# Optimization experiments

Hardware: AMD Instinct MI355X
Metric: run time of the kernel (lower is better)

The kernel has to match this reference:

```python
import jax, jax.numpy as jnp
import numpy as np

PRECS = 1e-6
# [min, max] scaling ranges for the 12 XAJ parameters (order matches parameters[:, i, :])
PARA_SCALE = [[0.3, 2.0], [0.0, 5.0], [0.01, 100.0], [0.01, 100.0], [0.01, 200.0],
              [0.09, 1.0], [0.01, 100.0], [0.0, 10.0], [0.01, 0.7], [0.01, 0.7],
              [0.0, 0.998], [0.0, 0.998]]


def setup_inputs() -> dict:
    key = jax.random.key(0)
    k1, k2 = jax.random.split(key)
    Nstep, Ngrid, mu = 365, 2000, 8
    # col 0 = P (mm/d), col 2 = PET (mm/d); col 1 unused by the model
    x = jax.random.uniform(k1, (Nstep, Ngrid, 3), dtype=jnp.float32) * 10.0
    parameters = jax.random.uniform(k2, (Ngrid, 12, mu), dtype=jnp.float32)
    return {"x": x, "parameters": parameters, "mu": mu}


def _xaj(x, parameters, mu):
    P = x[:, :, 0]          # [T, Ngrid]
    PET = x[:, :, 2]        # [T, Ngrid]  (index 2, matching the original code)
    Ngrid = x.shape[1]

    sc = lambda a, i: PARA_SCALE[i][0] + a * (PARA_SCALE[i][1] - PARA_SCALE[i][0])
    (parKE, parB, parWUM, parWLM, parWM, parC, parSM, parEX,
     parKI_, parKG_, parCI, parCG) = [sc(parameters[:, i, :], i) for i in range(12)]

    wdm = jnp.maximum(parWM - parWUM - parWLM, 0.0)
    sum_k = parKI_ + parKG_
    parKI = jnp.where(sum_k < 1.0, parKI_, (1.0 - PRECS) * parKI_ / (sum_k + PRECS))
    parKG = jnp.where(sum_k < 1.0, parKG_, (1.0 - PRECS) * parKG_ / (sum_k + PRECS))

    init_state = jnp.full((Ngrid, mu), 0.001, dtype=jnp.float32)
    WU0 = WL0 = WD0 = S0 = QI0 = QG0 = FR0_init = init_state

    def step(carry, inp):
        WU, WL, WD, S, FR0, QI, QG = carry
        P_row, PET_row = inp                      # each [Ngrid]
        P_t = P_row[:, None]                      # broadcast over mu
        PET_t = PET_row[:, None] * parKE

        # three-layer evapotranspiration
        EU = jnp.minimum(PET_t, WU + P_t)
        D = jnp.maximum(PET_t - EU, 0.0)
        wet_excess = jnp.maximum(WL - parC * parWLM, 0.0)
        wet_ratio = wet_excess / (wet_excess + 1.0)
        EL_wet = D * WL / (parWLM + PRECS)
        EL_dry = jnp.minimum(parC * D, WL)
        EL = jnp.maximum(wet_ratio * EL_wet + (1.0 - wet_ratio) * EL_dry, 0.0)
        EL = jnp.minimum(EL, WL)
        D_res = jnp.maximum(D - EL, 0.0)
        ED = jnp.minimum(parC * D_res, WD)
        E = EU + EL + ED

        # saturation-excess runoff
        PE = jnp.maximum(P_t - E, 0.0)
        W = WU + WL + WD
        WMM = parWM * (1.0 + parB)
        base_W = jnp.maximum(1.0 - W / (parWM + PRECS), PRECS)
        A = WMM * (1.0 - base_W ** (1.0 / (1.0 + parB)))
        ratio = jnp.minimum((PE + A) / (WMM + PRECS), 1.0)
        R_per = jnp.where(PE + A < WMM,
                          PE - (parWM - W) + parWM * (1.0 - ratio) ** (1.0 + parB),
                          PE - (parWM - W))
        R_per = jnp.maximum(R_per, 0.0)

        # soil moisture update (fill top-down, deplete top-down)
        dW = P_t - E - R_per
        dpos = jnp.maximum(dW, 0.0)
        fill_u = jnp.minimum(dpos, jnp.maximum(parWUM - WU, 0.0))
        WU = WU + fill_u; dpos = dpos - fill_u
        fill_l = jnp.minimum(dpos, jnp.maximum(parWLM - WL, 0.0))
        WL = WL + fill_l; dpos = dpos - fill_l
        fill_d = jnp.minimum(dpos, jnp.maximum(wdm - WD, 0.0))
        WD = WD + fill_d
        dneg = jnp.maximum(-dW, 0.0)
        sub_u = jnp.minimum(dneg, WU)
        WU = WU - sub_u; dneg = dneg - sub_u
        sub_l = jnp.minimum(dneg, WL)
        WL = WL - sub_l; dneg = dneg - sub_l
        sub_d = jnp.minimum(dneg, WD)
        WD = WD - sub_d

        # free-water reservoir + three-flow separation
        FR_new = R_per / (PE + PRECS)
        FR = jnp.where(PE > 0.0, FR_new, FR0)
        FR = jnp.clip(FR, 0.0, 1.0)
        S_eq = jnp.minimum(S * FR0 / (FR + PRECS), parSM)
        SMM = parSM * (1.0 + parEX)
        ratio_s = jnp.maximum(1.0 - S_eq / (parSM + PRECS), PRECS)
        AU = SMM * (1.0 - ratio_s ** (1.0 / (1.0 + parEX)))
        ratio_pa = jnp.minimum((PE + AU) / (SMM + PRECS), 1.0)
        RS1 = (PE + S_eq - parSM + parSM * (1.0 - ratio_pa) ** (1.0 + parEX)) * FR
        RS2 = (PE + S_eq - parSM) * FR
        RS = jnp.where(PE + AU < SMM, RS1, RS2)
        RS = jnp.minimum(jnp.maximum(RS, 0.0), R_per)
        S = jnp.minimum(S_eq + (R_per - RS) / (FR + PRECS), parSM)
        RI = parKI * S * FR
        RG = parKG * S * FR
        S = S * (1.0 - parKI - parKG)

        # linear reservoirs
        QI = parCI * QI + (1.0 - parCI) * RI
        QG = parCG * QG + (1.0 - parCG) * RG

        return (WU, WL, WD, S, FR, QI, QG), (RS, QI, QG, E)

    carry0 = (WU0, WL0, WD0, S0, FR0_init, QI0, QG0)
    _, (QS_inflow, QI_inflow, QG_inflow, ET_series) = jax.lax.scan(step, carry0, (P, PET))

    QSave = QS_inflow.mean(-1, keepdims=True)
    QIave = QI_inflow.mean(-1, keepdims=True)
    QGave = QG_inflow.mean(-1, keepdims=True)
    ETave = ET_series.mean(-1, keepdims=True)
    river_inflow = QS_inflow + QI_inflow + QG_inflow
    Qs = river_inflow.mean(-1, keepdims=True)   # muwts is None
    # [Nstep, Ngrid, 5]
    return jnp.concatenate([Qs, QSave, QIave, QGave, ETave], axis=-1)


def reference(x, parameters, mu):
    return _xaj(x, parameters, mu)
```

## Files before the change

### kernel.cpp

```cpp
#include <hip/hip_runtime.h>

#define PRECS 1e-6f

__device__ __forceinline__ float fpow(float b, float e) {
    return __builtin_amdgcn_exp2f(e * __builtin_amdgcn_logf(b));
}

__device__ __forceinline__ float frcp(float v) {
    return __builtin_amdgcn_rcpf(v);
}

template <int CTRL>
__device__ __forceinline__ float dpp_mov(float v) {
    return __int_as_float(
        __builtin_amdgcn_update_dpp(0, __float_as_int(v), CTRL, 0xF, 0xF, true));
}

__device__ __forceinline__ float rsum8(float v) {
    v += dpp_mov<0xB1>(v);
    v += dpp_mov<0x4E>(v);
    v += dpp_mov<0x141>(v);
    return v;
}

__global__ __launch_bounds__(192, 1) void xaj_kernel(
    const float* __restrict__ x,
    const float* __restrict__ prm,
    float* __restrict__ out)
{
    constexpr int Nstep = 365, Ngrid = 2000;
    constexpr int xstride = Ngrid * 3;
    constexpr int K = 16;
    constexpr int NBLK = 23;

    const int wid  = (int)threadIdx.x >> 6;
    const int lane = (int)threadIdx.x & 63;
    const int g = blockIdx.x * 8 + (lane >> 3);
    const int m = lane & 7;

    __shared__ float2 stIn[2][K][64];
    __shared__ float4 stA[2][K][64];
    __shared__ float4 stB[2][K][64];

    const float lo[12] = {0.3f,0.0f,0.01f,0.01f,0.01f,0.09f,0.01f,0.0f,0.01f,0.01f,0.0f,0.0f};
    const float hi[12] = {2.0f,5.0f,100.0f,100.0f,200.0f,1.0f,100.0f,10.0f,0.7f,0.7f,0.998f,0.998f};
    float p[12];
    const float* pb = prm + (size_t)g * 96 + m;
#pragma unroll
    for (int i = 0; i < 12; ++i)
        p[i] = lo[i] + pb[i * 8] * (hi[i] - lo[i]);

    const float KE=p[0], B=p[1], WUM=p[2], WLM=p[3], WM=p[4], C=p[5],
                SM=p[6], EX=p[7], KI_=p[8], KG_=p[9], CI=p[10], CG=p[11];

    const float wdm  = fmaxf(WM - WUM - WLM, 0.f);
    const float sumk = KI_ + KG_;
    const float nrm  = (1.f - PRECS) / (sumk + PRECS);
    const float KI   = (sumk < 1.f) ? KI_ : KI_ * nrm;
    const float KG   = (sumk < 1.f) ? KG_ : KG_ * nrm;
    const float expB = 1.f + B,  invB  = 1.f / expB;
    const float WMM  = WM * expB;
    const float expEX= 1.f + EX, invEX = 1.f / expEX;
    const float SMM  = SM * expEX;
    const float inv_WLM = 1.f / (WLM + PRECS);
    const float inv_WM  = 1.f / (WM  + PRECS);
    const float inv_WMM = 1.f / (WMM + PRECS);
    const float inv_SM  = 1.f / (SM  + PRECS);
    const float inv_SMM = 1.f / (SMM + PRECS);
    const float oneK = 1.f - KI - KG;
    const float omCI = 1.f - CI, omCG = 1.f - CG;
    const float CWLM = C * WLM;
    const float inv1p = 1.f / (1.f + PRECS);
    const float eps2  = fmaxf(PRECS, fmaf(-SM, inv_SM, 1.f));

    float WU = 0.001f, WL = 0.001f, WD = 0.001f;
    float S = 0.001f, FR0 = 0.001f;
    float iFR0 = frcp(FR0 + PRECS);
    float QI = 0.001f, QG = 0.001f;
    const float cKI = omCI * KI, cKG = omCG * KG;
    const float wa = (m == 0 || m == 1) ? 0.125f : 0.f;
    const float wb = (m == 0 || m == 2) ? 0.125f : 0.f;
    const float wc = (m == 0 || m == 3) ? 0.125f : 0.f;
    const float wd = (m >= 4) ? 0.125f : 0.f;
    const int   col = (m < 4) ? m : 4;
    float* outp = out + (size_t)g * 5 + col;
    const size_t ostr = (size_t)Ngrid * 5;
    const float* xg = x + (size_t)g * 3;
    float Pr[K], Er[K];

    auto ASTEP = [&](int buf) {
        float2 rin[K];
#pragma unroll
        for (int k = 0; k < K; ++k)
            rin[k] = stIn[buf][k][lane];
#pragma unroll
        for (int k = 0; k < K; ++k) {
            const float Pt = rin[k].x, PET_t = rin[k].y;
            const float EU = fminf(PET_t, WU + Pt);
            const float D  = fmaxf(PET_t - Pt - WU, 0.f);
            const float we = fmaxf(WL - CWLM, 0.f);
            const float wr = we * frcp(we + 1.f);
            const float cwet = wr * WL * inv_WLM;
            const float ELdry = fminf(C * D, WL);
            const float EL = fminf(fmaxf(fmaf(1.f - wr, ELdry, cwet * D), 0.f), WL);
            const float ED = fminf(C * fmaxf(D - EL, 0.f), WD);
            const float E  = EU + EL + ED;
            const float PE = fmaxf(Pt - E, 0.f);
            const float W = WU + WL + WD;
            const float base_W = fmaxf(fmaf(-W, inv_WM, 1.f), PRECS);
            const float pw1 = fpow(base_W, invB);
            const float omr = fmaxf(fmaf(-PE, inv_WMM, pw1), 0.f);
            const float R_per = fmaxf(fmaf(WM, fpow(omr, expB), PE + (W - WM)), 0.f);
            const float dW = Pt - E - R_per;
            const float capD = fmaxf(wdm, WD);
            const float cum0 = WU + dW;
            const float WUn  = __builtin_amdgcn_fmed3f(cum0, 0.f, WUM);
            const float cum1 = WL + (cum0 - WUn);
            const float WLn  = __builtin_amdgcn_fmed3f(cum1, 0.f, WLM);
            const float cum2 = WD + (cum1 - WLn);
            const float WDn  = __builtin_amdgcn_fmed3f(cum2, 0.f, capD);
            WU = WUn; WL = WLn; WD = WDn;
            stA[buf][k][lane] = make_float4(PE, R_per, E, 0.f);
        }
    };

    auto BSTEP = [&](int buf) {
        float4 ra[K];
#pragma unroll
        for (int k = 0; k < K; ++k)
            ra[k] = stA[buf][k][lane];
        float FRn[K], iFRn[K];
#pragma unroll
        for (int k = 0; k < K; ++k) {
            const float q  = frcp(ra[k].x + PRECS);
            const float aa = ra[k].y * q;
            FRn[k]  = fminf(aa, 1.f);
            iFRn[k] = fmaxf(frcp(aa + PRECS), inv1p);
        }
#pragma unroll
        for (int k = 0; k < K; ++k) {
            const float PE = ra[k].x, R_per = ra[k].y;
            const bool wet = PE > 0.f;
            const float FR  = wet ? FRn[k]  : FR0;
            const float iFR = wet ? iFRn[k] : iFR0;
            const float sf  = S * FR0;
            const float sf2 = sf * inv_SM;
            const float S_eq = fminf(sf * iFR, SM);
            const float ratio_s = fmaxf(fmaf(-sf2, iFR, 1.f), eps2);
            const float u   = fpow(ratio_s, invEX);
            const float om2 = fmaxf(fmaf(-PE, inv_SMM, u), 0.f);
            const float base = (PE - SM) + S_eq;
            float RS = fmaf(SM, fpow(om2, expEX), base) * FR;
            RS = __builtin_amdgcn_fmed3f(RS, 0.f, R_per);
            const float Sn = fminf(fmaf(R_per - RS, iFR, S_eq), SM);
            S  = Sn * oneK;
            FR0 = FR; iFR0 = iFR;
            stB[buf][k][lane] = make_float4(RS, FR * Sn, ra[k].z, 0.f);
        }
    };

    auto CISSUE = [&](int blk) {
#pragma unroll
        for (int k = 0; k < K; ++k) {
            int t = blk * K + k;
            t = (t < Nstep) ? t : Nstep - 1;
            const float* xq = xg + (size_t)t * xstride;
            Pr[k] = xq[0];
            Er[k] = xq[2];
        }
    };
    auto CWRITE = [&](int buf) {
#pragma unroll
        for (int k = 0; k < K; ++k)
            stIn[buf][k][lane] = make_float2(Pr[k], Er[k] * KE);
    };
    auto CRED = [&](int buf, int q) {
        float4 rb[K];
#pragma unroll
        for (int k = 0; k < K; ++k)
            rb[k] = stB[buf][k][lane];
        const int t0 = q * K;
#pragma unroll
        for (int k = 0; k < K; ++k) {
            QI = fmaf(CI, QI, cKI * rb[k].y);
            QG = fmaf(CG, QG, cKG * rb[k].y);
            const float u0 = rsum8(rb[k].x);
            const float u1 = rsum8(QI);
            const float u2 = rsum8(QG);
            const float u3 = rsum8(rb[k].z);
            const float v = fmaf(u0, wa, fmaf(u1, wb, fmaf(u2, wc, u3 * wd)));
            if (t0 + k < Nstep)
                outp[(size_t)(t0 + k) * ostr] = v;
        }
    };

    if (wid == 2) { CISSUE(0); CWRITE(0); }
    __syncthreads();

#pragma unroll 1
    for (int i = 0; i < 13; ++i) {
        const int p0 = 2 * i, p1 = 2 * i + 1;
        if (wid == 0) {
            if (p0 < NBLK) ASTEP(0);
        } else if (wid == 1) {
            if (p0 >= 1 && p0 <= NBLK) BSTEP(1);
        } else {
            const bool ld = (p0 + 1 < NBLK);
            if (ld) CISSUE(p0 + 1);
            if (p0 >= 2) CRED(0, p0 - 2);
            if (ld) CWRITE(1);
        }
        __syncthreads();
        if (wid == 0) {
            if (p1 < NBLK) ASTEP(1);
        } else if (wid == 1) {
            if (p1 <= NBLK) BSTEP(0);
        } else {
            const bool ld = (p1 + 1 < NBLK);
            if (ld) CISSUE(p1 + 1);
            if (p1 >= 2) CRED(1, p1 - 2);
            if (ld) CWRITE(0);
        }
        __syncthreads();
    }
}

extern "C" void kernel_launch(void* const* d_in, const int* in_sizes, int n_in,
                              void* d_out, int out_size, void* d_ws, size_t ws_size,
                              hipStream_t stream) {
    const float* x   = (const float*)d_in[0];
    const float* prm = (const float*)d_in[1];
    float* out = (float*)d_out;
    xaj_kernel<<<250, 192, 0, stream>>>(x, prm, out);
}
```

Measured before the change: 58.07 us.

## Split pipeline into four warp-specialized stages with dedicated FR precompute wave

Adds a fourth wavefront so the pipeline runs A (soil moisture), FR precompute plus input load, B (free water), and D (reservoir routing, reductions, stores) as separate stages. FR/iFR precomputation moves out of the serial B stage into the loader wave, and the output reduction moves to its own wave. This shortens the critical serial B stage. The cost is a deeper pipeline with more phases and a 4-deep stA buffer, more shared memory, and one more wave per block.

```diff
diff --git a/kernel.cpp b/kernel.cpp
--- a/kernel.cpp
+++ b/kernel.cpp
@@ -23,7 +23,7 @@
     return v;
 }
 
-__global__ __launch_bounds__(192, 1) void xaj_kernel(
+__global__ __launch_bounds__(256, 1) void xaj_kernel(
     const float* __restrict__ x,
     const float* __restrict__ prm,
     float* __restrict__ out)
@@ -32,6 +32,7 @@
     constexpr int xstride = Ngrid * 3;
     constexpr int K = 16;
     constexpr int NBLK = 23;
+    constexpr int NPH  = NBLK + 3;
 
     const int wid  = (int)threadIdx.x >> 6;
     const int lane = (int)threadIdx.x & 63;
@@ -39,8 +40,9 @@
     const int m = lane & 7;
 
     __shared__ float2 stIn[2][K][64];
-    __shared__ float4 stA[2][K][64];
-    __shared__ float4 stB[2][K][64];
+    __shared__ float4 stA[4][K][64];
+    __shared__ float2 stFR[2][K][64];
+    __shared__ float2 stB[2][K][64];
 
     const float lo[12] = {0.3f,0.0f,0.01f,0.01f,0.01f,0.09f,0.01f,0.0f,0.01f,0.01f,0.0f,0.0f};
     const float hi[12] = {2.0f,5.0f,100.0f,100.0f,200.0f,1.0f,100.0f,10.0f,0.7f,0.7f,0.998f,0.998f};
@@ -88,7 +90,7 @@
     const float* xg = x + (size_t)g * 3;
     float Pr[K], Er[K];
 
-    auto ASTEP = [&](int buf) {
+    auto ASTEP = [&](int buf, int obuf) {
         float2 rin[K];
 #pragma unroll
         for (int k = 0; k < K; ++k)
@@ -120,29 +122,23 @@
             const float cum2 = WD + (cum1 - WLn);
             const float WDn  = __builtin_amdgcn_fmed3f(cum2, 0.f, capD);
             WU = WUn; WL = WLn; WD = WDn;
-            stA[buf][k][lane] = make_float4(PE, R_per, E, 0.f);
-        }
-    };
-
-    auto BSTEP = [&](int buf) {
+            stA[obuf][k][lane] = make_float4(PE, R_per, E, 0.f);
+        }
+    };
+
+    auto BSTEP = [&](int abuf, int fbuf) {
         float4 ra[K];
-#pragma unroll
-        for (int k = 0; k < K; ++k)
-            ra[k] = stA[buf][k][lane];
-        float FRn[K], iFRn[K];
-#pragma unroll
-        for (int k = 0; k < K; ++k) {
-            const float q  = frcp(ra[k].x + PRECS);
-            const float aa = ra[k].y * q;
-            FRn[k]  = fminf(aa, 1.f);
-            iFRn[k] = fmaxf(frcp(aa + PRECS), inv1p);
-        }
+        float2 rf[K];
+#pragma unroll
+        for (int k = 0; k < K; ++k) ra[k] = stA[abuf][k][lane];
+#pragma unroll
+        for (int k = 0; k < K; ++k) rf[k] = stFR[fbuf][k][lane];
 #pragma unroll
         for (int k = 0; k < K; ++k) {
             const float PE = ra[k].x, R_per = ra[k].y;
             const bool wet = PE > 0.f;
-            const float FR  = wet ? FRn[k]  : FR0;
-            const float iFR = wet ? iFRn[k] : iFR0;
+            const float FR  = wet ? rf[k].x : FR0;
+            const float iFR = wet ? rf[k].y : iFR0;
             const float sf  = S * FR0;
             const float sf2 = sf * inv_SM;
             const float S_eq = fminf(sf * iFR, SM);
@@ -155,7 +151,7 @@
             const float Sn = fminf(fmaf(R_per - RS, iFR, S_eq), SM);
             S  = Sn * oneK;
             FR0 = FR; iFR0 = iFR;
-            stB[buf][k][lane] = make_float4(RS, FR * Sn, ra[k].z, 0.f);
+            stB[fbuf][k][lane] = make_float2(RS, FR * Sn);
         }
     };
 
@@ -169,17 +165,30 @@
             Er[k] = xq[2];
         }
     };
+    auto CFR = [&](int abuf, int fbuf) {
+#pragma unroll
+        for (int k = 0; k < K; ++k) {
+            const float4 ra = stA[abuf][k][lane];
+            const float q  = frcp(ra.x + PRECS);
+            const float aa = ra.y * q;
+            stFR[fbuf][k][lane] =
+                make_float2(fminf(aa, 1.f), fmaxf(frcp(aa + PRECS), inv1p));
+        }
+    };
     auto CWRITE = [&](int buf) {
 #pragma unroll
         for (int k = 0; k < K; ++k)
             stIn[buf][k][lane] = make_float2(Pr[k], Er[k] * KE);
     };
-    auto CRED = [&](int buf, int q) {
-        float4 rb[K];
-#pragma unroll
-        for (int k = 0; k < K; ++k)
-            rb[k] = stB[buf][k][lane];
-        const int t0 = q * K;
+
+    auto DSTEP = [&](int bbuf, int abuf, int blk) {
+        float2 rb[K];
+        float  re[K];
+#pragma unroll
+        for (int k = 0; k < K; ++k) rb[k] = stB[bbuf][k][lane];
+#pragma unroll
+        for (int k = 0; k < K; ++k) re[k] = stA[abuf][k][lane].z;
+        const int t0 = blk * K;
 #pragma unroll
         for (int k = 0; k < K; ++k) {
             QI = fmaf(CI, QI, cKI * rb[k].y);
@@ -187,7 +196,7 @@
             const float u0 = rsum8(rb[k].x);
             const float u1 = rsum8(QI);
             const float u2 = rsum8(QG);
-            const float u3 = rsum8(rb[k].z);
+            const float u3 = rsum8(re[k]);
             const float v = fmaf(u0, wa, fmaf(u1, wb, fmaf(u2, wc, u3 * wd)));
             if (t0 + k < Nstep)
                 outp[(size_t)(t0 + k) * ostr] = v;
@@ -198,28 +207,19 @@
     __syncthreads();
 
 #pragma unroll 1
-    for (int i = 0; i < 13; ++i) {
-        const int p0 = 2 * i, p1 = 2 * i + 1;
+    for (int ph = 0; ph < NPH; ++ph) {
         if (wid == 0) {
-            if (p0 < NBLK) ASTEP(0);
+            if (ph < NBLK) ASTEP(ph & 1, ph & 3);
         } else if (wid == 1) {
-            if (p0 >= 1 && p0 <= NBLK) BSTEP(1);
+            if (ph >= 2 && ph < NBLK + 2) BSTEP((ph - 2) & 3, (ph - 2) & 1);
+        } else if (wid == 2) {
+            const bool ld = (ph + 1 < NBLK);
+            if (ld) CISSUE(ph + 1);
+            if (ph >= 1 && ph < NBLK + 1)
+                CFR((ph - 1) & 3, (ph - 1) & 1);
+            if (ld) CWRITE((ph + 1) & 1);
         } else {
-            const bool ld = (p0 + 1 < NBLK);
-            if (ld) CISSUE(p0 + 1);
-            if (p0 >= 2) CRED(0, p0 - 2);
-            if (ld) CWRITE(1);
-        }
-        __syncthreads();
-        if (wid == 0) {
-            if (p1 < NBLK) ASTEP(1);
-        } else if (wid == 1) {
-            if (p1 <= NBLK) BSTEP(0);
-        } else {
-            const bool ld = (p1 + 1 < NBLK);
-            if (ld) CISSUE(p1 + 1);
-            if (p1 >= 2) CRED(1, p1 - 2);
-            if (ld) CWRITE(0);
+            if (ph >= 3) DSTEP((ph - 3) & 1, (ph - 3) & 3, ph - 3);
         }
         __syncthreads();
     }
@@ -231,5 +231,5 @@
     const float* x   = (const float*)d_in[0];
     const float* prm = (const float*)d_in[1];
     float* out = (float*)d_out;
-    xaj_kernel<<<250, 192, 0, stream>>>(x, prm, out);
-}
+    xaj_kernel<<<250, 256, 0, stream>>>(x, prm, out);
+}
```

After: 58.29 us. No clear change (+0.4%).
